# Kernel tuning notes

Measured on AMD Instinct MI355X. Metric: run time of the kernel, lower is better.

Reference implementation:

```python
import jax, jax.numpy as jnp
import numpy as np

GRID_SIZE = 5
NUM_BASES = 2 ** GRID_SIZE - 1  # 31: actual number of Haar bases produced by the loop

def _haar_edges():
    left, mid, right = [], [], []
    for level in range(GRID_SIZE):
        scale = 2 ** level
        for shift in range(scale):
            left.append(shift / scale)
            mid.append((shift + 0.5) / scale)
            right.append((shift + 1.0) / scale)
    return (np.asarray(left, np.float32), np.asarray(mid, np.float32), np.asarray(right, np.float32))

_LEFT, _MID, _RIGHT = _haar_edges()


def setup_inputs() -> dict:
    key = jax.random.key(0)
    k1, k2, k3 = jax.random.split(key, 3)
    B, IN, OUT = 16384, 256, 256
    x = jax.random.normal(k1, (B, IN), dtype=jnp.float32)
    base_weight = jax.random.normal(k2, (OUT, IN), dtype=jnp.float32) * 0.05
    spline_weight = jax.random.normal(k3, (OUT, IN, NUM_BASES), dtype=jnp.float32) * 0.05
    spline_scaler = jnp.ones((OUT, IN), dtype=jnp.float32)
    return {"x": x, "base_weight": base_weight, "spline_weight": spline_weight, "spline_scaler": spline_scaler}


def reference(x, base_weight, spline_weight, spline_scaler):
    # per-feature min/max normalization over the batch dim
    x_min = jnp.min(x, axis=0, keepdims=True)
    x_max = jnp.max(x, axis=0, keepdims=True)
    xn = (x - x_min) / (x_max - x_min + 1e-8)            # [B, IN]
    left = jnp.asarray(_LEFT, x.dtype)
    mid = jnp.asarray(_MID, x.dtype)
    right = jnp.asarray(_RIGHT, x.dtype)
    xe = xn[..., None]                                    # [B, IN, 1]
    mask1 = ((xe >= left) & (xe < mid)).astype(x.dtype)
    mask2 = ((xe >= mid) & (xe < right)).astype(x.dtype)
    bases = mask1 - mask2                                 # [B, IN, NB]
    base_out = jax.nn.relu(x) @ base_weight.T             # [B, OUT]
    sw = spline_weight * spline_scaler[..., None]         # [OUT, IN, NB]
    wavelet_out = jnp.einsum('bik,oik->bo', bases, sw)    # [B, OUT]
    return base_out + wavelet_out
```

## Files before the change

kernel.cpp:

```cpp
#include <hip/hip_runtime.h>
#include <stdint.h>

typedef short s16x8 __attribute__((ext_vector_type(8)));
typedef float f32x4 __attribute__((ext_vector_type(4)));

#define IN_F   256
#define OUT_F  256
#define BATCH  16384
#define NB     31
#define KONE   8192
#define KTOT   8448

typedef const __attribute__((address_space(1))) void* as1cvp;
typedef __attribute__((address_space(3))) void* as3vp;

__device__ __forceinline__ unsigned short f2bf(float f) {
    unsigned u = __float_as_uint(f);
    u += 0x7FFFu + ((u >> 16) & 1u);
    return (unsigned short)(u >> 16);
}

__global__ void minmax_part(const float* __restrict__ x,
                            float* __restrict__ pmn, float* __restrict__ pmx) {
    const int t = threadIdx.x;
    const int b0 = blockIdx.x * 32;
    float mn = 3.4e38f, mx = -3.4e38f;
    for (int r = 0; r < 32; ++r) {
        float v = x[(size_t)(b0 + r) * IN_F + t];
        mn = fminf(mn, v);
        mx = fmaxf(mx, v);
    }
    pmn[blockIdx.x * 256 + t] = mn;
    pmx[blockIdx.x * 256 + t] = mx;
}

__global__ __launch_bounds__(64) void minmax_reduce(
    const float* __restrict__ pmn, const float* __restrict__ pmx,
    float* __restrict__ xminF, float* __restrict__ rdenF) {
    const int j = blockIdx.x;
    const int lane = threadIdx.x;
    float mn = 3.4e38f, mx = -3.4e38f;
#pragma unroll
    for (int i = 0; i < 8; ++i) {
        int b = lane * 8 + i;
        mn = fminf(mn, pmn[(size_t)b * 256 + j]);
        mx = fmaxf(mx, pmx[(size_t)b * 256 + j]);
    }
#pragma unroll
    for (int off = 32; off; off >>= 1) {
        mn = fminf(mn, __shfl_down(mn, off));
        mx = fmaxf(mx, __shfl_down(mx, off));
    }
    if (lane == 0) {
        xminF[j] = mn;
        rdenF[j] = 1.0f / (mx - mn + 1e-8f);
    }
}

__global__ void build_wb(const float* __restrict__ bw, const float* __restrict__ sw,
                         const float* __restrict__ sc, unsigned short* __restrict__ Wb) {
    const int o = blockIdx.x;
    const int k0 = blockIdx.y * 2112;
    const int t = threadIdx.x;
    for (int k = k0 + t; k < k0 + 2112; k += 256) {
        float val;
        if (k < KONE) {
            int i = k >> 5, j = k & 31;
            float s = sc[o * IN_F + i];
            float acc = 0.f;
#pragma unroll
            for (int l = 0; l < 5; ++l) {
                int kk = (1 << l) - 1 + (j >> (5 - l));
                float w = sw[((size_t)(o * IN_F + i)) * NB + kk];
                acc += (((j >> (4 - l)) & 1) ? -w : w);
            }
            val = acc * s;
        } else {
            val = bw[o * IN_F + (k - KONE)];
        }
        Wb[(size_t)o * KTOT + k] = f2bf(val);
    }
}

__global__ __launch_bounds__(256) void leafk_t(
    const float* __restrict__ x, const float* __restrict__ xminF,
    const float* __restrict__ rdenF, unsigned char* __restrict__ lt) {
    __shared__ unsigned char lsh[256 * 68];
    const int t = threadIdx.x;
    const int b0 = blockIdx.x * 64;
    const float xmn = xminF[t], rdn = rdenF[t];
    for (int r = 0; r < 64; ++r) {
        float v = x[(size_t)(b0 + r) * IN_F + t];
        float xn = (v - xmn) * rdn;
        int l = (int)(xn * 32.0f);
        lsh[t * 68 + r] = (l >= 0 && l < 32) ? (unsigned char)l : (unsigned char)255;
    }
    __syncthreads();
    const int lane = t & 63, w = t >> 6;
    const unsigned* lshU = (const unsigned*)lsh;
#pragma unroll
    for (int ib = 0; ib < 16; ++ib) {
        int i = ib * 16 + w * 4 + (lane >> 4);
        unsigned val = lshU[i * 17 + (lane & 15)];
        *(unsigned*)(lt + (size_t)i * BATCH + b0 + (lane & 15) * 4) = val;
    }
}

__global__ __launch_bounds__(128, 4) void gemm_kan(
    const float* __restrict__ x,
    const unsigned short* __restrict__ Wb,
    const unsigned char* __restrict__ lt,
    float* __restrict__ out)
{
    __shared__ unsigned short Bsh[2 * 64 * 64];

    const int t     = threadIdx.x;
    const int lane  = t & 63;
    const int wv    = t >> 6;
    const int mtile = blockIdx.x;
    const int ntile = blockIdx.y;
    const int kbeg  = blockIdx.z * 66;
    const int kend  = kbeg + 66;

    const unsigned char* bbase = (const unsigned char*)(Wb
        + (size_t)(ntile * 64 + wv * 32 + (lane >> 3)) * KTOT
        + (((lane & 7) ^ (lane >> 3)) << 3));

    const int rr = lane & 15, kq = lane >> 4;
    const size_t lrow0 = (size_t)mtile * 64 + wv * 32 + rr;

    int boff[2][4];
#pragma unroll
    for (int ks = 0; ks < 2; ++ks)
#pragma unroll
        for (int nt = 0; nt < 4; ++nt) {
            int n = nt * 16 + rr, c = ks * 4 + kq;
            boff[ks][nt] = (n << 7) + ((c ^ (n & 7)) << 4);
        }

    {
        unsigned short* dst = Bsh + (kbeg & 1) * 4096 + wv * 2048;
        const unsigned char* src = bbase + (size_t)kbeg * 128;
#pragma unroll
        for (int q = 0; q < 4; ++q)
            __builtin_amdgcn_global_load_lds(
                (as1cvp)(src + (size_t)q * 8 * KTOT * 2),
                (as3vp)(uint32_t)(uintptr_t)(dst + q * 512), 16, 0, 0);
    }
    int lf[2][2];
#pragma unroll
    for (int ks = 0; ks < 2; ++ks)
#pragma unroll
        for (int mt = 0; mt < 2; ++mt)
            lf[ks][mt] = lt[(size_t)(kbeg * 2 + ks) * BATCH + lrow0 + mt * 16];
    __syncthreads();

    f32x4 acc[2][4] = {};

    for (int kb = kbeg; kb < kend; ++kb) {
        const int cur = kb & 1;

        if (kb + 1 < kend) {
            const unsigned char* src = bbase + (size_t)(kb + 1) * 128;
            unsigned short* dst = Bsh + (1 - cur) * 4096 + wv * 2048;
#pragma unroll
            for (int q = 0; q < 4; ++q)
                __builtin_amdgcn_global_load_lds(
                    (as1cvp)(src + (size_t)q * 8 * KTOT * 2),
                    (as3vp)(uint32_t)(uintptr_t)(dst + q * 512), 16, 0, 0);
        }

        s16x8 af[2][2];
        if (kb < 128) {
#pragma unroll
            for (int ks = 0; ks < 2; ++ks)
#pragma unroll
                for (int mt = 0; mt < 2; ++mt) {
                    int L = lf[ks][mt];
                    unsigned hot = ((L >> 3) == kq) ? (0x3F80u << ((L & 1) << 4)) : 0u;
                    int slot = (L >> 1) & 3;
                    union { s16x8 v; unsigned u[4]; } a;
                    a.u[0] = (slot == 0) ? hot : 0u;
                    a.u[1] = (slot == 1) ? hot : 0u;
                    a.u[2] = (slot == 2) ? hot : 0u;
                    a.u[3] = (slot == 3) ? hot : 0u;
                    af[ks][mt] = a.v;
                }
        } else {
#pragma unroll
            for (int ks = 0; ks < 2; ++ks)
#pragma unroll
                for (int mt = 0; mt < 2; ++mt) {
                    const float* xr = x + (lrow0 + mt * 16) * IN_F
                                        + (kb - 128) * 64 + ks * 32 + kq * 8;
                    union { s16x8 v; unsigned short s[8]; } a;
#pragma unroll
                    for (int e = 0; e < 8; ++e) a.s[e] = f2bf(fmaxf(xr[e], 0.0f));
                    af[ks][mt] = a.v;
                }
        }

        if (kb + 1 < kend && kb + 1 < 128) {
#pragma unroll
            for (int ks = 0; ks < 2; ++ks)
#pragma unroll
                for (int mt = 0; mt < 2; ++mt)
                    lf[ks][mt] = lt[(size_t)((kb + 1) * 2 + ks) * BATCH + lrow0 + mt * 16];
        }

        const char* bb = (const char*)Bsh + cur * 8192;
#pragma unroll
        for (int ks = 0; ks < 2; ++ks) {
            s16x8 bfr[4];
#pragma unroll
            for (int nt = 0; nt < 4; ++nt)
                bfr[nt] = *(const s16x8*)(bb + boff[ks][nt]);
#pragma unroll
            for (int mt = 0; mt < 2; ++mt)
#pragma unroll
                for (int nt = 0; nt < 4; ++nt)
                    acc[mt][nt] = __builtin_amdgcn_mfma_f32_16x16x32_bf16(
                        af[ks][mt], bfr[nt], acc[mt][nt], 0, 0, 0);
        }
        __syncthreads();
    }

    const int rq = lane >> 4;
#pragma unroll
    for (int mt = 0; mt < 2; ++mt)
#pragma unroll
        for (int nt = 0; nt < 4; ++nt)
#pragma unroll
            for (int v = 0; v < 4; ++v) {
                int row = mtile * 64 + wv * 32 + mt * 16 + rq * 4 + v;
                int col = ntile * 64 + nt * 16 + rr;
                atomicAdd(&out[(size_t)row * OUT_F + col], acc[mt][nt][v]);
            }
}

extern "C" void kernel_launch(void* const* d_in, const int* in_sizes, int n_in,
                              void* d_out, int out_size, void* d_ws, size_t ws_size,
                              hipStream_t stream) {
    (void)in_sizes; (void)n_in; (void)out_size; (void)ws_size;
    const float* x  = (const float*)d_in[0];
    const float* bw = (const float*)d_in[1];
    const float* sw = (const float*)d_in[2];
    const float* sc = (const float*)d_in[3];
    float* out = (float*)d_out;

    char* ws = (char*)d_ws;
    unsigned short* Wb   = (unsigned short*)ws;
    unsigned char*  lt   = (unsigned char*)(ws + 4325376);
    float* pmn   = (float*)(ws + 4325376);
    float* pmx   = (float*)(ws + 4325376 + 524288);
    float* xminF = (float*)(ws + 8519680);
    float* rdenF = (float*)(ws + 8520704);

    hipMemsetAsync(out, 0, (size_t)BATCH * OUT_F * 4, stream);

    minmax_part<<<512, 256, 0, stream>>>(x, pmn, pmx);
    minmax_reduce<<<256, 64, 0, stream>>>(pmn, pmx, xminF, rdenF);
    build_wb<<<dim3(256, 4), 256, 0, stream>>>(bw, sw, sc, Wb);
    leafk_t<<<256, 256, 0, stream>>>(x, xminF, rdenF, lt);
    gemm_kan<<<dim3(256, 4, 2), 128, 0, stream>>>(x, Wb, lt, out);
}
```

Before: 178.4 us.

## Enlarge GEMM M-tile, row-major leaf indices, remap blocks, and register-cache spline weights

The GEMM now uses 256-thread blocks covering 128 rows, so each staged 64-column B tile is shared by four waves instead of two. The grid is flattened with a swizzled block-id mapping, and the K split changes to 68/64. Leaf indices are stored row-major, so each wave loads eight bytes of leaf codes per four K-blocks instead of byte loads from a transposed table. The leaf kernel drops its LDS transpose and uses float4 loads. build_wb loads the 31 spline weights into registers once per thread and writes packed 16-byte stores, removing repeated gathers. In exchange, the GEMM kernel has higher register pressure, fewer blocks, and an uneven K split.

```diff
diff --git a/kernel.cpp b/kernel.cpp
--- a/kernel.cpp
+++ b/kernel.cpp
@@ -3,6 +3,7 @@
 
 typedef short s16x8 __attribute__((ext_vector_type(8)));
 typedef float f32x4 __attribute__((ext_vector_type(4)));
+typedef unsigned long long u64;
 
 #define IN_F   256
 #define OUT_F  256
@@ -57,56 +58,62 @@
     }
 }
 
-__global__ void build_wb(const float* __restrict__ bw, const float* __restrict__ sw,
-                         const float* __restrict__ sc, unsigned short* __restrict__ Wb) {
-    const int o = blockIdx.x;
-    const int k0 = blockIdx.y * 2112;
-    const int t = threadIdx.x;
-    for (int k = k0 + t; k < k0 + 2112; k += 256) {
-        float val;
-        if (k < KONE) {
-            int i = k >> 5, j = k & 31;
-            float s = sc[o * IN_F + i];
+__global__ __launch_bounds__(256) void build_wb(
+    const float* __restrict__ bw, const float* __restrict__ sw,
+    const float* __restrict__ sc, unsigned short* __restrict__ Wb) {
+    const int o = blockIdx.x, i = threadIdx.x;
+    const float s = sc[o * IN_F + i];
+    const float* swp = sw + (size_t)(o * IN_F + i) * NB;
+    float w[NB];
+#pragma unroll
+    for (int k = 0; k < NB; ++k) w[k] = swp[k];
+    unsigned short* dst = Wb + (size_t)o * KTOT + i * 32;
+#pragma unroll
+    for (int q = 0; q < 4; ++q) {
+        union { s16x8 v; unsigned short s8[8]; } pk;
+#pragma unroll
+        for (int e = 0; e < 8; ++e) {
+            int j = q * 8 + e;
             float acc = 0.f;
 #pragma unroll
             for (int l = 0; l < 5; ++l) {
                 int kk = (1 << l) - 1 + (j >> (5 - l));
-                float w = sw[((size_t)(o * IN_F + i)) * NB + kk];
-                acc += (((j >> (4 - l)) & 1) ? -w : w);
-            }
-            val = acc * s;
-        } else {
-            val = bw[o * IN_F + (k - KONE)];
-        }
-        Wb[(size_t)o * KTOT + k] = f2bf(val);
-    }
-}
-
-__global__ __launch_bounds__(256) void leafk_t(
+                acc += (((j >> (4 - l)) & 1) ? -w[kk] : w[kk]);
+            }
+            pk.s8[e] = f2bf(acc * s);
+        }
+        *(s16x8*)(dst + q * 8) = pk.v;
+    }
+    Wb[(size_t)o * KTOT + KONE + i] = f2bf(bw[o * IN_F + i]);
+}
+
+__global__ __launch_bounds__(256) void leafk(
     const float* __restrict__ x, const float* __restrict__ xminF,
     const float* __restrict__ rdenF, unsigned char* __restrict__ lt) {
-    __shared__ unsigned char lsh[256 * 68];
-    const int t = threadIdx.x;
+    const int lane = threadIdx.x & 63, w = threadIdx.x >> 6;
     const int b0 = blockIdx.x * 64;
-    const float xmn = xminF[t], rdn = rdenF[t];
-    for (int r = 0; r < 64; ++r) {
-        float v = x[(size_t)(b0 + r) * IN_F + t];
-        float xn = (v - xmn) * rdn;
-        int l = (int)(xn * 32.0f);
-        lsh[t * 68 + r] = (l >= 0 && l < 32) ? (unsigned char)l : (unsigned char)255;
-    }
-    __syncthreads();
-    const int lane = t & 63, w = t >> 6;
-    const unsigned* lshU = (const unsigned*)lsh;
-#pragma unroll
-    for (int ib = 0; ib < 16; ++ib) {
-        int i = ib * 16 + w * 4 + (lane >> 4);
-        unsigned val = lshU[i * 17 + (lane & 15)];
-        *(unsigned*)(lt + (size_t)i * BATCH + b0 + (lane & 15) * 4) = val;
-    }
-}
-
-__global__ __launch_bounds__(128, 4) void gemm_kan(
+    const float4 mn = *(const float4*)(xminF + lane * 4);
+    const float4 rd = *(const float4*)(rdenF + lane * 4);
+#pragma unroll 4
+    for (int r = 0; r < 16; ++r) {
+        int row = b0 + w * 16 + r;
+        float4 v = *(const float4*)(x + (size_t)row * IN_F + lane * 4);
+        unsigned b[4];
+        float xs[4] = {v.x, v.y, v.z, v.w};
+        float ms[4] = {mn.x, mn.y, mn.z, mn.w};
+        float rs[4] = {rd.x, rd.y, rd.z, rd.w};
+#pragma unroll
+        for (int e = 0; e < 4; ++e) {
+            float xn = (xs[e] - ms[e]) * rs[e];
+            int l = (int)(xn * 32.0f);
+            b[e] = (l >= 0 && l < 32) ? (unsigned)l : 255u;
+        }
+        unsigned pk = b[0] | (b[1] << 8) | (b[2] << 16) | (b[3] << 24);
+        *(unsigned*)(lt + (size_t)row * IN_F + lane * 4) = pk;
+    }
+}
+
+__global__ __launch_bounds__(256, 4) void gemm_kan(
     const float* __restrict__ x,
     const unsigned short* __restrict__ Wb,
     const unsigned char* __restrict__ lt,
@@ -114,20 +121,26 @@
 {
     __shared__ unsigned short Bsh[2 * 64 * 64];
 
-    const int t     = threadIdx.x;
-    const int lane  = t & 63;
-    const int wv    = t >> 6;
-    const int mtile = blockIdx.x;
-    const int ntile = blockIdx.y;
-    const int kbeg  = blockIdx.z * 66;
-    const int kend  = kbeg + 66;
+    const int t    = threadIdx.x;
+    const int lane = t & 63;
+    const int wv   = t >> 6;
+
+    const int bid   = blockIdx.x;
+    const int sid   = (bid & 7) * 128 + (bid >> 3);
+    const int mtile = sid & 127;
+    const int ntile = (sid >> 7) & 3;
+    const int zz    = sid >> 9;
+    const int kbeg  = zz ? 68 : 0;
+    const int kend  = zz ? 132 : 68;
 
     const unsigned char* bbase = (const unsigned char*)(Wb
-        + (size_t)(ntile * 64 + wv * 32 + (lane >> 3)) * KTOT
+        + (size_t)(ntile * 64 + wv * 16 + (lane >> 3)) * KTOT
         + (((lane & 7) ^ (lane >> 3)) << 3));
 
     const int rr = lane & 15, kq = lane >> 4;
-    const size_t lrow0 = (size_t)mtile * 64 + wv * 32 + rr;
+    const int r0 = mtile * 128 + wv * 32 + rr;
+    const unsigned char* lp0 = lt + (size_t)r0 * IN_F;
+    const unsigned char* lp1 = lt + (size_t)(r0 + 16) * IN_F;
 
     int boff[2][4];
 #pragma unroll
@@ -139,90 +152,90 @@
         }
 
     {
-        unsigned short* dst = Bsh + (kbeg & 1) * 4096 + wv * 2048;
         const unsigned char* src = bbase + (size_t)kbeg * 128;
-#pragma unroll
-        for (int q = 0; q < 4; ++q)
+        unsigned short* dst = Bsh + (kbeg & 1) * 4096 + wv * 1024;
+#pragma unroll
+        for (int qq = 0; qq < 2; ++qq)
             __builtin_amdgcn_global_load_lds(
-                (as1cvp)(src + (size_t)q * 8 * KTOT * 2),
-                (as3vp)(uint32_t)(uintptr_t)(dst + q * 512), 16, 0, 0);
-    }
-    int lf[2][2];
-#pragma unroll
-    for (int ks = 0; ks < 2; ++ks)
-#pragma unroll
-        for (int mt = 0; mt < 2; ++mt)
-            lf[ks][mt] = lt[(size_t)(kbeg * 2 + ks) * BATCH + lrow0 + mt * 16];
+                (as1cvp)(src + (size_t)qq * 8 * KTOT * 2),
+                (as3vp)(uint32_t)(uintptr_t)(dst + qq * 512), 16, 0, 0);
+    }
+    u64 L0 = *(const u64*)(lp0 + 2 * kbeg);
+    u64 L1 = *(const u64*)(lp1 + 2 * kbeg);
     __syncthreads();
 
     f32x4 acc[2][4] = {};
 
-    for (int kb = kbeg; kb < kend; ++kb) {
-        const int cur = kb & 1;
-
-        if (kb + 1 < kend) {
-            const unsigned char* src = bbase + (size_t)(kb + 1) * 128;
-            unsigned short* dst = Bsh + (1 - cur) * 4096 + wv * 2048;
-#pragma unroll
-            for (int q = 0; q < 4; ++q)
-                __builtin_amdgcn_global_load_lds(
-                    (as1cvp)(src + (size_t)q * 8 * KTOT * 2),
-                    (as3vp)(uint32_t)(uintptr_t)(dst + q * 512), 16, 0, 0);
-        }
-
-        s16x8 af[2][2];
-        if (kb < 128) {
-#pragma unroll
-            for (int ks = 0; ks < 2; ++ks)
-#pragma unroll
-                for (int mt = 0; mt < 2; ++mt) {
-                    int L = lf[ks][mt];
-                    unsigned hot = ((L >> 3) == kq) ? (0x3F80u << ((L & 1) << 4)) : 0u;
-                    int slot = (L >> 1) & 3;
-                    union { s16x8 v; unsigned u[4]; } a;
-                    a.u[0] = (slot == 0) ? hot : 0u;
-                    a.u[1] = (slot == 1) ? hot : 0u;
-                    a.u[2] = (slot == 2) ? hot : 0u;
-                    a.u[3] = (slot == 3) ? hot : 0u;
-                    af[ks][mt] = a.v;
-                }
-        } else {
-#pragma unroll
-            for (int ks = 0; ks < 2; ++ks)
-#pragma unroll
-                for (int mt = 0; mt < 2; ++mt) {
-                    const float* xr = x + (lrow0 + mt * 16) * IN_F
-                                        + (kb - 128) * 64 + ks * 32 + kq * 8;
-                    union { s16x8 v; unsigned short s[8]; } a;
-#pragma unroll
-                    for (int e = 0; e < 8; ++e) a.s[e] = f2bf(fmaxf(xr[e], 0.0f));
-                    af[ks][mt] = a.v;
-                }
-        }
-
-        if (kb + 1 < kend && kb + 1 < 128) {
-#pragma unroll
-            for (int ks = 0; ks < 2; ++ks)
+    for (int kb0 = kbeg; kb0 < kend; kb0 += 4) {
+        u64 nL0 = L0, nL1 = L1;
+        if (kb0 + 4 < kend && kb0 + 4 < 128) {
+            nL0 = *(const u64*)(lp0 + 2 * (kb0 + 4));
+            nL1 = *(const u64*)(lp1 + 2 * (kb0 + 4));
+        }
+        const bool denseg = (kb0 >= 128);
+#pragma unroll
+        for (int j = 0; j < 4; ++j) {
+            const int kb = kb0 + j;
+            const int cur = kb & 1;
+
+            if (kb + 1 < kend) {
+                const unsigned char* src = bbase + (size_t)(kb + 1) * 128;
+                unsigned short* dst = Bsh + (1 - cur) * 4096 + wv * 1024;
+#pragma unroll
+                for (int qq = 0; qq < 2; ++qq)
+                    __builtin_amdgcn_global_load_lds(
+                        (as1cvp)(src + (size_t)qq * 8 * KTOT * 2),
+                        (as3vp)(uint32_t)(uintptr_t)(dst + qq * 512), 16, 0, 0);
+            }
+
+            s16x8 af[2][2];
+            if (!denseg) {
+#pragma unroll
+                for (int ks = 0; ks < 2; ++ks)
+#pragma unroll
+                    for (int mt = 0; mt < 2; ++mt) {
+                        const u64 Lw = mt ? L1 : L0;
+                        const int L = (int)((Lw >> (((j << 1) | ks) << 3)) & 255u);
+                        unsigned hot = ((L >> 3) == kq) ? (0x3F80u << ((L & 1) << 4)) : 0u;
+                        int slot = (L >> 1) & 3;
+                        union { s16x8 v; unsigned u[4]; } a;
+                        a.u[0] = (slot == 0) ? hot : 0u;
+                        a.u[1] = (slot == 1) ? hot : 0u;
+                        a.u[2] = (slot == 2) ? hot : 0u;
+                        a.u[3] = (slot == 3) ? hot : 0u;
+                        af[ks][mt] = a.v;
+                    }
+            } else {
+#pragma unroll
+                for (int ks = 0; ks < 2; ++ks)
+#pragma unroll
+                    for (int mt = 0; mt < 2; ++mt) {
+                        const float* xr = x + (size_t)(r0 + mt * 16) * IN_F
+                                            + (kb - 128) * 64 + ks * 32 + kq * 8;
+                        union { s16x8 v; unsigned short s8[8]; } a;
+#pragma unroll
+                        for (int e = 0; e < 8; ++e) a.s8[e] = f2bf(fmaxf(xr[e], 0.0f));
+                        af[ks][mt] = a.v;
+                    }
+            }
+
+            const char* bb = (const char*)Bsh + cur * 8192;
+#pragma unroll
+            for (int ks = 0; ks < 2; ++ks) {
+                s16x8 bfr[4];
+#pragma unroll
+                for (int nt = 0; nt < 4; ++nt)
+                    bfr[nt] = *(const s16x8*)(bb + boff[ks][nt]);
 #pragma unroll
                 for (int mt = 0; mt < 2; ++mt)
-                    lf[ks][mt] = lt[(size_t)((kb + 1) * 2 + ks) * BATCH + lrow0 + mt * 16];
-        }
-
-        const char* bb = (const char*)Bsh + cur * 8192;
-#pragma unroll
-        for (int ks = 0; ks < 2; ++ks) {
-            s16x8 bfr[4];
-#pragma unroll
-            for (int nt = 0; nt < 4; ++nt)
-                bfr[nt] = *(const s16x8*)(bb + boff[ks][nt]);
-#pragma unroll
-            for (int mt = 0; mt < 2; ++mt)
-#pragma unroll
-                for (int nt = 0; nt < 4; ++nt)
-                    acc[mt][nt] = __builtin_amdgcn_mfma_f32_16x16x32_bf16(
-                        af[ks][mt], bfr[nt], acc[mt][nt], 0, 0, 0);
-        }
-        __syncthreads();
+#pragma unroll
+                    for (int nt = 0; nt < 4; ++nt)
+                        acc[mt][nt] = __builtin_amdgcn_mfma_f32_16x16x32_bf16(
+                            af[ks][mt], bfr[nt], acc[mt][nt], 0, 0, 0);
+            }
+            __syncthreads();
+        }
+        L0 = nL0; L1 = nL1;
     }
 
     const int rq = lane >> 4;
@@ -232,7 +245,7 @@
         for (int nt = 0; nt < 4; ++nt)
 #pragma unroll
             for (int v = 0; v < 4; ++v) {
-                int row = mtile * 64 + wv * 32 + mt * 16 + rq * 4 + v;
+                int row = mtile * 128 + wv * 32 + mt * 16 + rq * 4 + v;
                 int col = ntile * 64 + nt * 16 + rr;
                 atomicAdd(&out[(size_t)row * OUT_F + col], acc[mt][nt][v]);
             }
@@ -260,7 +273,7 @@
 
     minmax_part<<<512, 256, 0, stream>>>(x, pmn, pmx);
     minmax_reduce<<<256, 64, 0, stream>>>(pmn, pmx, xminF, rdenF);
-    build_wb<<<dim3(256, 4), 256, 0, stream>>>(bw, sw, sc, Wb);
-    leafk_t<<<256, 256, 0, stream>>>(x, xminF, rdenF, lt);
-    gemm_kan<<<dim3(256, 4, 2), 128, 0, stream>>>(x, Wb, lt, out);
-}
+    build_wb<<<256, 256, 0, stream>>>(bw, sw, sc, Wb);
+    leafk<<<256, 256, 0, stream>>>(x, xminF, rdenF, lt);
+    gemm_kan<<<1024, 256, 0, stream>>>(x, Wb, lt, out);
+}
```

Result: no change. 175.6 us (-1.6%).
